# Performance work log

Hardware: AMD Instinct MI355X
Metric: run time of the kernel (lower is better)

## Reference

```python
import jax, jax.numpy as jnp
import numpy as np

TOP_K = 2  # top-k experts per token


def setup_inputs() -> dict:
    key = jax.random.key(0)
    k1, k2, k3, k4, k5 = jax.random.split(key, 5)
    B, S, D = 1, 2048, 2048
    E, F = 8, 1408
    scale = 0.02
    return {
        "hidden_states": jax.random.normal(k1, (B, S, D), dtype=jnp.float32),
        "gate_w": jax.random.normal(k2, (E, D), dtype=jnp.float32) * scale,
        "w_gate": jax.random.normal(k3, (E, D, F), dtype=jnp.float32) * scale,
        "w_up": jax.random.normal(k4, (E, D, F), dtype=jnp.float32) * scale,
        "w_down": jax.random.normal(k5, (E, F, D), dtype=jnp.float32) * scale,
    }


def reference(hidden_states, gate_w, w_gate, w_up, w_down):
    B, S, D = hidden_states.shape
    T = B * S
    x = hidden_states.reshape(T, D)  # flatten tokens, as in forward()

    # Router: combined gate built from per-rank 1-row gates -> [T, E] logits
    router_logits = jnp.einsum("td,ed->te", x, gate_w)
    routing_weights = jax.nn.softmax(router_logits, axis=-1)
    top_w, top_idx = jax.lax.top_k(routing_weights, TOP_K)  # [T, K]

    # Per-token combine weight for each expert (0 if expert not selected).
    # Equivalent to the one_hot expert_mask + index_add combine in the module.
    comb = jnp.zeros((T, gate_w.shape[0]), dtype=routing_weights.dtype)
    comb = comb.at[jnp.arange(T)[:, None], top_idx].add(top_w)  # [T, E]

    # Each expert is a Qwen2 MLP: down(silu(gate(x)) * up(x)).
    # (Dispatch/all-to-all collapses to dense-per-expert + masked combine
    #  on a single device; tokens with comb==0 contribute nothing.)
    g = jnp.einsum("td,edf->etf", x, w_gate)
    u = jnp.einsum("td,edf->etf", x, w_up)
    y = jnp.einsum("etf,efd->etd", jax.nn.silu(g) * u, w_down)  # [E, T, D]

    out = jnp.einsum("te,etd->td", comb, y)  # weighted combine (index_add)
    return out.reshape(B, S, D)
```

## Files before the change

kernel.cpp:

```cpp
#include <hip/hip_runtime.h>
#include <stdint.h>


#define TT 2048
#define DD 2048
#define FF 1408
#define NE 8
#define HROWS 5120
#define TRASH (2*TT)

typedef float f32x4 __attribute__((ext_vector_type(4)));
typedef short bf16x8 __attribute__((ext_vector_type(8)));

__device__ __forceinline__ unsigned short f2bf(float f) {
    unsigned int x = __float_as_uint(f);
    return (unsigned short)((x + 0x7fffu + ((x >> 16) & 1u)) >> 16);
}
__device__ __forceinline__ float bf2f(unsigned short u) {
    union { unsigned int i; float f; } v; v.i = ((unsigned int)u) << 16; return v.f;
}
__device__ __forceinline__ uint4 cvt8(float4 a, float4 b) {
    uint4 o; unsigned short* po = (unsigned short*)&o;
    po[0] = f2bf(a.x); po[1] = f2bf(a.y); po[2] = f2bf(a.z); po[3] = f2bf(a.w);
    po[4] = f2bf(b.x); po[5] = f2bf(b.y); po[6] = f2bf(b.z); po[7] = f2bf(b.w);
    return o;
}
__device__ __forceinline__ void gld16(const void* g, void* l) {
    __builtin_amdgcn_global_load_lds((const __attribute__((address_space(1))) void*)g,
                                     (__attribute__((address_space(3))) void*)l, 16, 0, 0);
}

__global__ void convert_x_kernel(const float* __restrict__ x,
                                 unsigned short* __restrict__ xb) {
    const size_t i = ((size_t)blockIdx.x * 256 + threadIdx.x) * 8;
    float4 a = ((const float4*)(x + i))[0];
    float4 b = ((const float4*)(x + i))[1];
    *(uint4*)(xb + i) = cvt8(a, b);
}

__device__ __forceinline__ void transpose_tile(const float* __restrict__ src,
                                               unsigned short* __restrict__ dst,
                                               int R, int C, int r0, int c0) {
    __shared__ unsigned short tile[64][65];
    const int tid = threadIdx.x;
    const int lr = tid >> 3;
    const int lc = (tid & 7) * 8;
#pragma unroll
    for (int p = 0; p < 2; ++p) {
        int rr = lr + p * 32;
        const float* sp = &src[(size_t)(r0 + rr) * C + c0 + lc];
        float4 a = ((const float4*)sp)[0];
        float4 b = ((const float4*)sp)[1];
        uint4 v = cvt8(a, b);
        const unsigned short* pv = (const unsigned short*)&v;
#pragma unroll
        for (int i = 0; i < 8; ++i) tile[rr][lc + i] = pv[i];
    }
    __syncthreads();
#pragma unroll
    for (int p = 0; p < 2; ++p) {
        int cc = lr + p * 32;
        uint4 o; unsigned short* po = (unsigned short*)&o;
#pragma unroll
        for (int i = 0; i < 8; ++i) po[i] = tile[lc + i][cc];
        *(uint4*)&dst[(size_t)(c0 + cc) * R + r0 + lc] = o;
    }
}

__global__ void transpose_gu_kernel(const float* __restrict__ wg,
                                    const float* __restrict__ wu,
                                    unsigned short* __restrict__ WgT,
                                    unsigned short* __restrict__ WuT) {
    const int z = blockIdx.z;
    const float* src; unsigned short* dst;
    if (z < 8) { src = wg + (size_t)z * DD * FF;       dst = WgT + (size_t)z * FF * DD; }
    else       { src = wu + (size_t)(z - 8) * DD * FF; dst = WuT + (size_t)(z - 8) * FF * DD; }
    transpose_tile(src, dst, DD, FF, blockIdx.y * 64, blockIdx.x * 64);
}

__global__ void transpose_d_kernel(const float* __restrict__ wd,
                                   unsigned short* __restrict__ WdT) {
    const int z = blockIdx.z;
    transpose_tile(wd + (size_t)z * FF * DD, WdT + (size_t)z * DD * FF,
                   FF, DD, blockIdx.y * 64, blockIdx.x * 64);
}

__global__ void router_kernel(const float* __restrict__ x,
                              const float* __restrict__ gw,
                              int* __restrict__ cnt,
                              int* __restrict__ tok,
                              float* __restrict__ wtv,
                              int* __restrict__ dstv) {
    const int wv = threadIdx.x >> 6, lane = threadIdx.x & 63;
    const int t = blockIdx.x * 4 + wv;
    float acc[NE];
#pragma unroll
    for (int e = 0; e < NE; ++e) acc[e] = 0.f;
    const float* xr = x + (size_t)t * DD;
    for (int j = lane; j < DD; j += 64) {
        float xv = xr[j];
#pragma unroll
        for (int e = 0; e < NE; ++e) acc[e] += xv * gw[e * DD + j];
    }
#pragma unroll
    for (int e = 0; e < NE; ++e) {
        float v = acc[e];
        v += __shfl_xor(v, 32); v += __shfl_xor(v, 16); v += __shfl_xor(v, 8);
        v += __shfl_xor(v, 4);  v += __shfl_xor(v, 2);  v += __shfl_xor(v, 1);
        acc[e] = v;
    }
    if (lane == 0) {
        float mx = acc[0];
#pragma unroll
        for (int e = 1; e < NE; ++e) mx = fmaxf(mx, acc[e]);
        float p[NE], s = 0.f;
#pragma unroll
        for (int e = 0; e < NE; ++e) { p[e] = __expf(acc[e] - mx); s += p[e]; }
        int i0 = 0;
#pragma unroll
        for (int e = 1; e < NE; ++e) if (p[e] > p[i0]) i0 = e;
        int i1 = (i0 == 0) ? 1 : 0;
#pragma unroll
        for (int e = 0; e < NE; ++e) if (e != i0 && p[e] > p[i1]) i1 = e;
        float inv = 1.f / s;
        int p0 = atomicAdd(&cnt[i0], 1);
        tok[i0 * TT + p0] = t; wtv[i0 * TT + p0] = p[i0] * inv; dstv[i0 * TT + p0] = 2 * t;
        int p1 = atomicAdd(&cnt[i1], 1);
        tok[i1 * TT + p1] = t; wtv[i1 * TT + p1] = p[i1] * inv; dstv[i1 * TT + p1] = 2 * t + 1;
    }
}

__global__ void finalize_kernel(const int* __restrict__ cnt,
                                int* __restrict__ base,
                                int* __restrict__ cntpad,
                                int* __restrict__ tok,
                                float* __restrict__ wtv,
                                int* __restrict__ dstv) {
    __shared__ int sc[NE], sp[NE];
    if (threadIdx.x == 0) {
        int b = 0;
        for (int e = 0; e < NE; ++e) {
            int c = cnt[e]; int pd = (c + 127) & ~127;
            base[e] = b; cntpad[e] = pd; sc[e] = c; sp[e] = pd; b += pd;
        }
    }
    __syncthreads();
    for (int e = 0; e < NE; ++e)
        for (int i = sc[e] + (int)threadIdx.x; i < sp[e]; i += 256) {
            tok[e * TT + i] = 0; wtv[e * TT + i] = 0.f; dstv[e * TT + i] = TRASH;
        }
}

__launch_bounds__(256, 2)
__global__ void gemm1_kernel(const unsigned short* __restrict__ Xb,
                             const unsigned short* __restrict__ WgT,
                             const unsigned short* __restrict__ WuT,
                             const int* __restrict__ tok,
                             const int* __restrict__ base,
                             const int* __restrict__ cntpad,
                             unsigned short* __restrict__ H) {
    __shared__ unsigned short As[128 * 32];
    __shared__ unsigned short Bg[64 * 32];
    __shared__ unsigned short Bu[64 * 32];
    __shared__ int s_tok[128];

    const int e = blockIdx.z, rb = blockIdx.y, fb = blockIdx.x;
    const int cp = cntpad[e];
    if (rb * 128 >= cp) return;
    const int b0 = base[e];

    const int tid = threadIdx.x;
    if (tid < 128) s_tok[tid] = tok[e * TT + rb * 128 + tid];
    __syncthreads();

    const int w = tid >> 6, lane = tid & 63;
    const int r = lane & 15, q = lane >> 4;
    const int wm = w & 1, wn = w >> 1;

    const int arow = w * 32 + (lane >> 2);
    const int brow = w * 16 + (lane >> 2);
    const int koff = (lane & 3) * 8;
    const unsigned short* ga0 = Xb + (size_t)s_tok[arow] * DD + koff;
    const unsigned short* ga1 = Xb + (size_t)s_tok[arow + 16] * DD + koff;
    const size_t wb = (size_t)e * FF * DD + (size_t)(fb * 64 + brow) * DD + koff;
    const unsigned short* gg = WgT + wb;
    const unsigned short* gu = WuT + wb;
    unsigned short* la0 = As + arow * 32 + koff;
    unsigned short* la1 = la0 + 16 * 32;
    unsigned short* lg  = Bg + brow * 32 + koff;
    unsigned short* lu  = Bu + brow * 32 + koff;

    f32x4 accg[4][2] = {};
    f32x4 accu[4][2] = {};

    for (int kt = 0; kt < DD / 32; ++kt) {
        gld16(ga0, la0); gld16(ga1, la1);
        gld16(gg, lg);   gld16(gu, lu);
        ga0 += 32; ga1 += 32; gg += 32; gu += 32;
        __syncthreads();
        bf16x8 af[4], gf[2], uf[2];
#pragma unroll
        for (int m = 0; m < 4; ++m)
            af[m] = *(const bf16x8*)&As[(wm * 64 + m * 16 + r) * 32 + q * 8];
#pragma unroll
        for (int n = 0; n < 2; ++n) {
            gf[n] = *(const bf16x8*)&Bg[(wn * 32 + n * 16 + r) * 32 + q * 8];
            uf[n] = *(const bf16x8*)&Bu[(wn * 32 + n * 16 + r) * 32 + q * 8];
        }
#pragma unroll
        for (int m = 0; m < 4; ++m)
#pragma unroll
            for (int n = 0; n < 2; ++n) {
                accg[m][n] = __builtin_amdgcn_mfma_f32_16x16x32_bf16(af[m], gf[n], accg[m][n], 0, 0, 0);
                accu[m][n] = __builtin_amdgcn_mfma_f32_16x16x32_bf16(af[m], uf[n], accu[m][n], 0, 0, 0);
            }
        __syncthreads();
    }

    const size_t hr0 = (size_t)(b0 + rb * 128 + wm * 64);
#pragma unroll
    for (int m = 0; m < 4; ++m)
#pragma unroll
        for (int n = 0; n < 2; ++n)
#pragma unroll
            for (int rr = 0; rr < 4; ++rr) {
                float g = accg[m][n][rr], u = accu[m][n][rr];
                float h = (g / (1.f + __expf(-g))) * u;
                int row = m * 16 + q * 4 + rr;
                int col = fb * 64 + wn * 32 + n * 16 + r;
                H[(hr0 + row) * FF + col] = f2bf(h);
            }
}

__launch_bounds__(256, 2)
__global__ void gemm2_kernel(const unsigned short* __restrict__ H,
                             const unsigned short* __restrict__ WdT,
                             const float* __restrict__ wtv,
                             const int* __restrict__ dstv,
                             const int* __restrict__ base,
                             const int* __restrict__ cntpad,
                             unsigned short* __restrict__ Y) {
    __shared__ unsigned short As[128 * 32];
    __shared__ unsigned short Bs[64 * 32];
    __shared__ float s_w[128];
    __shared__ int s_d[128];

    const int e = blockIdx.z, rb = blockIdx.y, db = blockIdx.x;
    const int cp = cntpad[e];
    if (rb * 128 >= cp) return;
    const int b0 = base[e];

    const int tid = threadIdx.x;
    if (tid < 128) {
        int idx = e * TT + rb * 128 + tid;
        s_w[tid] = wtv[idx]; s_d[tid] = dstv[idx];
    }
    __syncthreads();

    const int w = tid >> 6, lane = tid & 63;
    const int r = lane & 15, q = lane >> 4;
    const int wm = w & 1, wn = w >> 1;

    const int arow = w * 32 + (lane >> 2);
    const int brow = w * 16 + (lane >> 2);
    const int koff = (lane & 3) * 8;
    const unsigned short* ga0 = H + (size_t)(b0 + rb * 128 + arow) * FF + koff;
    const unsigned short* ga1 = ga0 + (size_t)16 * FF;
    const unsigned short* gb = WdT + (size_t)e * DD * FF + (size_t)(db * 64 + brow) * FF + koff;
    unsigned short* la0 = As + arow * 32 + koff;
    unsigned short* la1 = la0 + 16 * 32;
    unsigned short* lb  = Bs + brow * 32 + koff;

    f32x4 acc[4][2] = {};

    for (int kt = 0; kt < FF / 32; ++kt) {
        gld16(ga0, la0); gld16(ga1, la1); gld16(gb, lb);
        ga0 += 32; ga1 += 32; gb += 32;
        __syncthreads();
        bf16x8 af[4], bf[2];
#pragma unroll
        for (int m = 0; m < 4; ++m)
            af[m] = *(const bf16x8*)&As[(wm * 64 + m * 16 + r) * 32 + q * 8];
#pragma unroll
        for (int n = 0; n < 2; ++n)
            bf[n] = *(const bf16x8*)&Bs[(wn * 32 + n * 16 + r) * 32 + q * 8];
#pragma unroll
        for (int m = 0; m < 4; ++m)
#pragma unroll
            for (int n = 0; n < 2; ++n)
                acc[m][n] = __builtin_amdgcn_mfma_f32_16x16x32_bf16(af[m], bf[n], acc[m][n], 0, 0, 0);
        __syncthreads();
    }

#pragma unroll
    for (int m = 0; m < 4; ++m)
#pragma unroll
        for (int n = 0; n < 2; ++n)
#pragma unroll
            for (int rr = 0; rr < 4; ++rr) {
                int row = wm * 64 + m * 16 + q * 4 + rr;
                int col = db * 64 + wn * 32 + n * 16 + r;
                float v = s_w[row] * acc[m][n][rr];
                Y[(size_t)s_d[row] * DD + col] = f2bf(v);
            }
}

__global__ void combine_kernel(const unsigned short* __restrict__ Y,
                               float* __restrict__ out) {
    const int t = blockIdx.x;
    const int d = threadIdx.x * 8;
    uint4 a = *(const uint4*)(Y + (size_t)(2 * t) * DD + d);
    uint4 b = *(const uint4*)(Y + (size_t)(2 * t + 1) * DD + d);
    const unsigned short* pa = (const unsigned short*)&a;
    const unsigned short* pb = (const unsigned short*)&b;
    float4 o0, o1;
    o0.x = bf2f(pa[0]) + bf2f(pb[0]);  o0.y = bf2f(pa[1]) + bf2f(pb[1]);
    o0.z = bf2f(pa[2]) + bf2f(pb[2]);  o0.w = bf2f(pa[3]) + bf2f(pb[3]);
    o1.x = bf2f(pa[4]) + bf2f(pb[4]);  o1.y = bf2f(pa[5]) + bf2f(pb[5]);
    o1.z = bf2f(pa[6]) + bf2f(pb[6]);  o1.w = bf2f(pa[7]) + bf2f(pb[7]);
    float* op = out + (size_t)t * DD + d;
    ((float4*)op)[0] = o0;
    ((float4*)op)[1] = o1;
}

extern "C" void kernel_launch(void* const* d_in, const int* in_sizes, int n_in,
                              void* d_out, int out_size, void* d_ws, size_t ws_size,
                              hipStream_t stream) {
    const float* x      = (const float*)d_in[0];
    const float* gw     = (const float*)d_in[1];
    const float* w_gate = (const float*)d_in[2];
    const float* w_up   = (const float*)d_in[3];
    const float* w_down = (const float*)d_in[4];
    float* out = (float*)d_out;

    uint8_t* ws = (uint8_t*)d_ws;
    size_t off = 0;
    auto alloc = [&](size_t bytes) -> void* {
        void* p = ws + off;
        off = (off + bytes + 255) & ~(size_t)255;
        return p;
    };
    int*   cnt    = (int*)  alloc(NE * 4);
    int*   basep  = (int*)  alloc(NE * 4);
    int*   cntpad = (int*)  alloc(NE * 4);
    int*   tok    = (int*)  alloc((size_t)NE * TT * 4);
    float* wtv    = (float*)alloc((size_t)NE * TT * 4);
    int*   dstv   = (int*)  alloc((size_t)NE * TT * 4);
    unsigned short* Xb  = (unsigned short*)alloc((size_t)TT * DD * 2);
    unsigned short* Hb  = (unsigned short*)alloc((size_t)HROWS * FF * 2);
    unsigned short* Yb  = (unsigned short*)alloc((size_t)(2 * TT + 8) * DD * 2);
    unsigned short* WT  = (unsigned short*)alloc((size_t)2 * NE * FF * DD * 2);
    unsigned short* WgT = WT;
    unsigned short* WuT = WT + (size_t)NE * FF * DD;
    unsigned short* WdT = WT;
    (void)ws_size; (void)in_sizes; (void)n_in; (void)out_size;

    hipMemsetAsync(cnt, 0, NE * 4, stream);
    convert_x_kernel<<<dim3(TT * DD / 2048), 256, 0, stream>>>(x, Xb);
    transpose_gu_kernel<<<dim3(22, 32, 16), 256, 0, stream>>>(w_gate, w_up, WgT, WuT);
    router_kernel<<<dim3(TT / 4), 256, 0, stream>>>(x, gw, cnt, tok, wtv, dstv);
    finalize_kernel<<<1, 256, 0, stream>>>(cnt, basep, cntpad, tok, wtv, dstv);
    gemm1_kernel<<<dim3(FF / 64, TT / 128, NE), 256, 0, stream>>>(Xb, WgT, WuT, tok, basep, cntpad, Hb);
    transpose_d_kernel<<<dim3(32, 22, 8), 256, 0, stream>>>(w_down, WdT);
    gemm2_kernel<<<dim3(DD / 64, TT / 128, NE), 256, 0, stream>>>(Hb, WdT, wtv, dstv, basep, cntpad, Yb);
    combine_kernel<<<dim3(TT), 256, 0, stream>>>(Yb, out);
}
```

Measured before the change: 528.9 us.

## Transpose weights in registers and fuse x bf16 conversion into router

Replaces the LDS-based 64x64 transpose with a register-only 8x8-per-lane transpose over 128x128 tiles. Each lane reads eight rows of eight floats and writes eight transposed bf16 vectors, which removes the shared-memory round trip and the barrier. It also folds the fp32-to-bf16 conversion of x into the router kernel and vectorises the router loads, so x is read once and one launch is dropped. In exchange, the transpose's global reads and writes are strided per lane, which may coalesce less well and uses more registers per thread.

After: 530.0 us. No clear change (+0.2%).

```diff
diff --git a/kernel.cpp b/kernel.cpp
--- a/kernel.cpp
+++ b/kernel.cpp
@@ -19,51 +19,35 @@
 __device__ __forceinline__ float bf2f(unsigned short u) {
     union { unsigned int i; float f; } v; v.i = ((unsigned int)u) << 16; return v.f;
 }
-__device__ __forceinline__ uint4 cvt8(float4 a, float4 b) {
-    uint4 o; unsigned short* po = (unsigned short*)&o;
-    po[0] = f2bf(a.x); po[1] = f2bf(a.y); po[2] = f2bf(a.z); po[3] = f2bf(a.w);
-    po[4] = f2bf(b.x); po[5] = f2bf(b.y); po[6] = f2bf(b.z); po[7] = f2bf(b.w);
-    return o;
-}
 __device__ __forceinline__ void gld16(const void* g, void* l) {
     __builtin_amdgcn_global_load_lds((const __attribute__((address_space(1))) void*)g,
                                      (__attribute__((address_space(3))) void*)l, 16, 0, 0);
 }
 
-__global__ void convert_x_kernel(const float* __restrict__ x,
-                                 unsigned short* __restrict__ xb) {
-    const size_t i = ((size_t)blockIdx.x * 256 + threadIdx.x) * 8;
-    float4 a = ((const float4*)(x + i))[0];
-    float4 b = ((const float4*)(x + i))[1];
-    *(uint4*)(xb + i) = cvt8(a, b);
-}
-
-__device__ __forceinline__ void transpose_tile(const float* __restrict__ src,
-                                               unsigned short* __restrict__ dst,
-                                               int R, int C, int r0, int c0) {
-    __shared__ unsigned short tile[64][65];
-    const int tid = threadIdx.x;
-    const int lr = tid >> 3;
-    const int lc = (tid & 7) * 8;
-#pragma unroll
-    for (int p = 0; p < 2; ++p) {
-        int rr = lr + p * 32;
-        const float* sp = &src[(size_t)(r0 + rr) * C + c0 + lc];
-        float4 a = ((const float4*)sp)[0];
-        float4 b = ((const float4*)sp)[1];
-        uint4 v = cvt8(a, b);
-        const unsigned short* pv = (const unsigned short*)&v;
-#pragma unroll
-        for (int i = 0; i < 8; ++i) tile[rr][lc + i] = pv[i];
-    }
-    __syncthreads();
-#pragma unroll
-    for (int p = 0; p < 2; ++p) {
-        int cc = lr + p * 32;
-        uint4 o; unsigned short* po = (unsigned short*)&o;
-#pragma unroll
-        for (int i = 0; i < 8; ++i) po[i] = tile[lc + i][cc];
-        *(uint4*)&dst[(size_t)(c0 + cc) * R + r0 + lc] = o;
+__device__ __forceinline__ void treg(const float* __restrict__ src,
+                                     unsigned short* __restrict__ dst,
+                                     int R, int C, int r0, int c0) {
+    const int lane = threadIdx.x & 63, w = threadIdx.x >> 6;
+    const int bi = lane >> 3, bj = lane & 7;
+    const int sr = r0 + (w & 1) * 64 + bi * 8;
+    const int sc = c0 + (w >> 1) * 64 + bj * 8;
+    float4 fa[8], fb[8];
+#pragma unroll
+    for (int k = 0; k < 8; ++k) {
+        const float* p = src + (size_t)(sr + k) * C + sc;
+        fa[k] = ((const float4*)p)[0];
+        fb[k] = ((const float4*)p)[1];
+    }
+#pragma unroll
+    for (int k = 0; k < 8; ++k) {
+        uint4 ov; unsigned short* po = (unsigned short*)&ov;
+#pragma unroll
+        for (int l = 0; l < 8; ++l) {
+            float v = (k < 4) ? ((const float*)&fa[l])[k]
+                              : ((const float*)&fb[l])[k - 4];
+            po[l] = f2bf(v);
+        }
+        *(uint4*)&dst[(size_t)(sc + k) * R + sr] = ov;
     }
 }
 
@@ -75,14 +59,14 @@
     const float* src; unsigned short* dst;
     if (z < 8) { src = wg + (size_t)z * DD * FF;       dst = WgT + (size_t)z * FF * DD; }
     else       { src = wu + (size_t)(z - 8) * DD * FF; dst = WuT + (size_t)(z - 8) * FF * DD; }
-    transpose_tile(src, dst, DD, FF, blockIdx.y * 64, blockIdx.x * 64);
+    treg(src, dst, DD, FF, blockIdx.y * 128, blockIdx.x * 128);
 }
 
 __global__ void transpose_d_kernel(const float* __restrict__ wd,
                                    unsigned short* __restrict__ WdT) {
     const int z = blockIdx.z;
-    transpose_tile(wd + (size_t)z * FF * DD, WdT + (size_t)z * DD * FF,
-                   FF, DD, blockIdx.y * 64, blockIdx.x * 64);
+    treg(wd + (size_t)z * FF * DD, WdT + (size_t)z * DD * FF,
+         FF, DD, blockIdx.y * 128, blockIdx.x * 128);
 }
 
 __global__ void router_kernel(const float* __restrict__ x,
@@ -90,17 +74,28 @@
                               int* __restrict__ cnt,
                               int* __restrict__ tok,
                               float* __restrict__ wtv,
-                              int* __restrict__ dstv) {
+                              int* __restrict__ dstv,
+                              unsigned short* __restrict__ xb) {
     const int wv = threadIdx.x >> 6, lane = threadIdx.x & 63;
     const int t = blockIdx.x * 4 + wv;
     float acc[NE];
 #pragma unroll
     for (int e = 0; e < NE; ++e) acc[e] = 0.f;
     const float* xr = x + (size_t)t * DD;
-    for (int j = lane; j < DD; j += 64) {
-        float xv = xr[j];
-#pragma unroll
-        for (int e = 0; e < NE; ++e) acc[e] += xv * gw[e * DD + j];
+    unsigned short* xbr = xb + (size_t)t * DD;
+#pragma unroll
+    for (int it = 0; it < DD / 256; ++it) {
+        const int j = it * 256 + lane * 4;
+        float4 xv = *(const float4*)(xr + j);
+        short4 o;
+        o.x = (short)f2bf(xv.x); o.y = (short)f2bf(xv.y);
+        o.z = (short)f2bf(xv.z); o.w = (short)f2bf(xv.w);
+        *(short4*)(xbr + j) = o;
+#pragma unroll
+        for (int e = 0; e < NE; ++e) {
+            float4 g = *(const float4*)(gw + e * DD + j);
+            acc[e] += xv.x * g.x + xv.y * g.y + xv.z * g.z + xv.w * g.w;
+        }
     }
 #pragma unroll
     for (int e = 0; e < NE; ++e) {
@@ -356,12 +351,11 @@
     (void)ws_size; (void)in_sizes; (void)n_in; (void)out_size;
 
     hipMemsetAsync(cnt, 0, NE * 4, stream);
-    convert_x_kernel<<<dim3(TT * DD / 2048), 256, 0, stream>>>(x, Xb);
-    transpose_gu_kernel<<<dim3(22, 32, 16), 256, 0, stream>>>(w_gate, w_up, WgT, WuT);
-    router_kernel<<<dim3(TT / 4), 256, 0, stream>>>(x, gw, cnt, tok, wtv, dstv);
+    transpose_gu_kernel<<<dim3(11, 16, 16), 256, 0, stream>>>(w_gate, w_up, WgT, WuT);
+    router_kernel<<<dim3(TT / 4), 256, 0, stream>>>(x, gw, cnt, tok, wtv, dstv, Xb);
     finalize_kernel<<<1, 256, 0, stream>>>(cnt, basep, cntpad, tok, wtv, dstv);
     gemm1_kernel<<<dim3(FF / 64, TT / 128, NE), 256, 0, stream>>>(Xb, WgT, WuT, tok, basep, cntpad, Hb);
-    transpose_d_kernel<<<dim3(32, 22, 8), 256, 0, stream>>>(w_down, WdT);
+    transpose_d_kernel<<<dim3(16, 11, 8), 256, 0, stream>>>(w_down, WdT);
     gemm2_kernel<<<dim3(DD / 64, TT / 128, NE), 256, 0, stream>>>(Hb, WdT, wtv, dstv, basep, cntpad, Yb);
     combine_kernel<<<dim3(TT), 256, 0, stream>>>(Yb, out);
 }
```
